# Kernel tuning notes

Hardware: AMD Instinct MI355X
Metric: run time of the kernel (lower is better)

The kernel has to match this reference:

```python
import jax, jax.numpy as jnp
import numpy as np

B, S, H, K = 16, 1024, 1024, 256


def _span(x, Ws, bs, start, end):
    # x: [B,S,H]; start/end: [B,K] int indices into the S axis
    def proj(W, b):
        return jnp.einsum('bsh,oh->bso', x, W) + b  # nn.Linear: x @ W.T + b

    def gather(p, idx):
        # batched index_select along seq axis -> [B,K,H]
        return jnp.take_along_axis(p, idx[..., None], axis=1)

    p1, p2, p3, p4 = (proj(W, b) for W, b in zip(Ws, bs))
    span = (gather(p1, start) + gather(p2, end)
            + (gather(p3, start) - gather(p3, end))
            + gather(p4, start) * gather(p4, end))
    return jnp.tanh(span)


def setup_inputs() -> dict:
    key = jax.random.key(0)
    ks = jax.random.split(key, 20)
    inp = {
        'hidden_states': jax.random.normal(ks[0], (B, S, H), dtype=jnp.float32),
        'prem_word_idxs': jax.random.randint(ks[1], (B, 1, 2, K), 0, S, dtype=jnp.int64) if jax.config.read('jax_enable_x64') else jax.random.randint(ks[1], (B, 1, 2, K), 0, S).astype(jnp.int32),
        'hypo_word_idxs': jax.random.randint(ks[2], (B, 1, 2, K), 0, S).astype(jnp.int32),
    }
    names = ['Wp1', 'bp1', 'Wp2', 'bp2', 'Wp3', 'bp3', 'Wp4', 'bp4',
             'Wh1', 'bh1', 'Wh2', 'bh2', 'Wh3', 'bh3', 'Wh4', 'bh4']
    for i, n in enumerate(names):
        k = ks[3 + i]
        if n.startswith('W'):
            inp[n] = jax.random.normal(k, (H, H), dtype=jnp.float32) * 0.02
        else:
            inp[n] = jax.random.normal(k, (H,), dtype=jnp.float32) * 0.02
    return inp


def reference(hidden_states, prem_word_idxs, hypo_word_idxs,
              Wp1, bp1, Wp2, bp2, Wp3, bp3, Wp4, bp4,
              Wh1, bh1, Wh2, bh2, Wh3, bh3, Wh4, bh4):
    p_idx = prem_word_idxs[:, 0]  # squeeze(1) -> [B,2,K]
    h_idx = hypo_word_idxs[:, 0]
    prem_h_ij = _span(hidden_states, (Wp1, Wp2, Wp3, Wp4), (bp1, bp2, bp3, bp4),
                      p_idx[:, 0], p_idx[:, 1])
    hypo_h_ij = _span(hidden_states, (Wh1, Wh2, Wh3, Wh4), (bh1, bh2, bh3, bh4),
                      h_idx[:, 0], h_idx[:, 1])
    return (prem_h_ij, hypo_h_ij)
```

## Files before the change

kernel.cpp:

```cpp
#include <hip/hip_runtime.h>
#include <hip/hip_bf16.h>

typedef _Float16 f16;
typedef _Float16 f16x4 __attribute__((ext_vector_type(4)));
typedef _Float16 f16x8 __attribute__((ext_vector_type(8)));
typedef float    f32x4 __attribute__((ext_vector_type(4)));

#define H_DIM 1024
#define S_DIM 1024
#define PLANE (1024*1024)
#define MT 128
#define NT 64
#define KT 32
#define AP (MT*KT)
#define ABUF (2*AP)
#define XOFF (6*PLANE)

__device__ __forceinline__ void load_lds16(const f16* g, f16* l) {
    __builtin_amdgcn_global_load_lds(
        (const __attribute__((address_space(1))) void*)g,
        (__attribute__((address_space(3))) void*)l, 16, 0, 0);
}

__global__ __launch_bounds__(256) void prep_w(
    const float* __restrict__ Wp1, const float* __restrict__ Wp2,
    const float* __restrict__ Wp3, const float* __restrict__ Wp4,
    const float* __restrict__ Wh1, const float* __restrict__ Wh2,
    const float* __restrict__ Wh3, const float* __restrict__ Wh4,
    f16* __restrict__ ws)
{
    const int tid  = blockIdx.x * 256 + threadIdx.x;
    const int span = tid >> 18;
    const size_t i = (size_t)(tid & 262143) * 4;
    const float* W1 = span ? Wh1 : Wp1;
    const float* W2 = span ? Wh2 : Wp2;
    const float* W3 = span ? Wh3 : Wp3;
    const float* W4 = span ? Wh4 : Wp4;
    f16* base = ws + (size_t)span * 3 * PLANE;

    f32x4 w1 = *(const f32x4*)(W1 + i);
    f32x4 w2 = *(const f32x4*)(W2 + i);
    f32x4 w3 = *(const f32x4*)(W3 + i);
    f32x4 w4 = *(const f32x4*)(W4 + i);

    f16x4 wa, wb, wc;
#pragma unroll
    for (int j = 0; j < 4; ++j) {
        wa[j] = (f16)(w1[j] + w3[j]);
        wb[j] = (f16)(w2[j] - w3[j]);
        wc[j] = (f16)w4[j];
    }
    *(f16x4*)(base + 0*PLANE + i) = wa;
    *(f16x4*)(base + 1*PLANE + i) = wb;
    *(f16x4*)(base + 2*PLANE + i) = wc;
}

#define XPREP_T (4096*256)
__global__ __launch_bounds__(256) void prep_x(
    const float* __restrict__ x, f16* __restrict__ ws)
{
    const int tid = blockIdx.x * 256 + threadIdx.x;
#pragma unroll
    for (int it = 0; it < 4; ++it) {
        const size_t i = ((size_t)(it * XPREP_T + tid)) * 4;
        f32x4 v = *(const f32x4*)(x + i);
        f16x4 h;
#pragma unroll
        for (int j = 0; j < 4; ++j) h[j] = (f16)v[j];
        *(f16x4*)(ws + XOFF + i) = h;
    }
}

#define K_STEP(FB, FA, WCNT, FIN)                                              \
  {                                                                            \
    f16x8 afr0[4], afr1[4], bfrg[6];                                           \
    const f16* Ab = &A_all[rbA];                                               \
    _Pragma("unroll")                                                          \
    for (int mf = 0; mf < 4; ++mf) {                                           \
      int r = (wm + mf * 16 + lrow) * KT + lqs * 8;                            \
      afr0[mf] = *(const f16x8*)&Ab[r];                                        \
      afr1[mf] = *(const f16x8*)&Ab[AP + r];                                   \
    }                                                                          \
    _Pragma("unroll")                                                          \
    for (int j = 0; j < 6; ++j) {                                              \
      int p = j >> 1, nf = j & 1;                                              \
      bfrg[j] = *(const f16x8*)&B_lds[p * 2048 + (wn + nf * 16 + lrow) * KT + lqs * 8]; \
    }                                                                          \
    if (!(FIN)) {                                                              \
      __asm__ volatile("s_waitcnt lgkmcnt(0)" ::: "memory");                   \
      __builtin_amdgcn_s_barrier();                                            \
      if (FB) {                                                                \
        _Pragma("unroll")                                                      \
        for (int j = 0; j < 3; ++j) { load_lds16(bq[j], &B_lds[bdst[j]]); bq[j] += KT; } \
      }                                                                        \
      if (FA) {                                                                \
        f16* dst = &A_all[wbA];                                                \
        _Pragma("unroll")                                                      \
        for (int j = 0; j < 4; ++j) { load_lds16(ap[j], dst + adst[j]); ap[j] += KT; } \
      }                                                                        \
    }                                                                          \
    _Pragma("unroll")                                                          \
    for (int mf = 0; mf < 4; ++mf)                                             \
      _Pragma("unroll")                                                        \
      for (int nf = 0; nf < 2; ++nf) {                                         \
        accL[mf][nf] = __builtin_amdgcn_mfma_f32_16x16x32_f16(afr0[mf], bfrg[0*2+nf], accL[mf][nf], 0,0,0); \
        accL[mf][nf] = __builtin_amdgcn_mfma_f32_16x16x32_f16(afr1[mf], bfrg[1*2+nf], accL[mf][nf], 0,0,0); \
        accP[mf][nf] = __builtin_amdgcn_mfma_f32_16x16x32_f16(afr0[mf], bfrg[2*2+nf], accP[mf][nf], 0,0,0); \
        accQ[mf][nf] = __builtin_amdgcn_mfma_f32_16x16x32_f16(afr1[mf], bfrg[2*2+nf], accQ[mf][nf], 0,0,0); \
      }                                                                        \
    if (!(FIN)) {                                                              \
      __asm__ volatile("s_waitcnt vmcnt(" #WCNT ")" ::: "memory");             \
      __builtin_amdgcn_s_barrier();                                            \
      rbA = (rbA == 2 * ABUF) ? 0 : rbA + ABUF;                                \
      wbA = (wbA == 2 * ABUF) ? 0 : wbA + ABUF;                                \
    }                                                                          \
  }

__global__ __launch_bounds__(256) void span_gemm(
    const f16* __restrict__ xh,
    const int* __restrict__ idxP, const int* __restrict__ idxH,
    const f16* __restrict__ wpl,
    const float* __restrict__ bp1, const float* __restrict__ bp2, const float* __restrict__ bp4,
    const float* __restrict__ bh1, const float* __restrict__ bh2, const float* __restrict__ bh4,
    float* __restrict__ out)
{
    const int t     = threadIdx.x;
    const int mtile = blockIdx.x;
    const int ntile = blockIdx.y;
    const int span  = blockIdx.z;

    const int* idx   = span ? idxH : idxP;
    const f16* wbase = wpl + (size_t)span * 3 * PLANE;
    const float* b1 = span ? bh1 : bp1;
    const float* b2 = span ? bh2 : bp2;
    const float* b4 = span ? bh4 : bp4;
    float* obase = out + (size_t)span * 4096 * H_DIM;

    __shared__ __align__(16) f16 A_all[3 * ABUF];
    __shared__ __align__(16) f16 B_lds[3 * NT * KT];

    int* rowoff = (int*)A_all;
    {
        int side = t >> 7, m = t & 127;
        int bk = mtile * MT + m;
        int b  = bk >> 8, kk = bk & 255;
        rowoff[side * 128 + m] = (b * S_DIM + idx[b * 512 + side * 256 + kk]) * H_DIM;
    }
    __syncthreads();

    const int wid  = t >> 6;
    const int lane = t & 63;
    const int wm   = (wid & 1) * 64;
    const int wn   = (wid >> 1) * 32;
    const int lrow = lane & 15;
    const int lq   = lane >> 4;
    const int lqs  = lq ^ ((lrow >> 1) & 3);

    const int schunk = (lane & 3) ^ ((lane >> 3) & 3);

    const f16* ap[4]; int adst[4];
#pragma unroll
    for (int j = 0; j < 4; ++j) {
        int o = wid * 4 + j;
        int p = o >> 3, g = o & 7;
        int r = g * 16 + (lane >> 2);
        ap[j]   = xh + rowoff[p * 128 + r] + schunk * 8;
        adst[j] = p * AP + g * 16 * KT;
    }
    __syncthreads();

    const f16* bq[3]; int bdst[3];
#pragma unroll
    for (int j = 0; j < 3; ++j) {
        int o = wid * 3 + j;
        int p = o >> 2, g = o & 3;
        int grow = ntile * NT + g * 16 + (lane >> 2);
        bq[j]   = wbase + (size_t)p * PLANE + (size_t)grow * H_DIM + schunk * 8;
        bdst[j] = p * 2048 + g * 16 * KT;
    }

    f32x4 accL[4][2], accP[4][2], accQ[4][2];
    {
        f32x4 z = {0.f, 0.f, 0.f, 0.f};
#pragma unroll
        for (int mf = 0; mf < 4; ++mf)
#pragma unroll
            for (int nf = 0; nf < 2; ++nf) { accL[mf][nf] = z; accP[mf][nf] = z; accQ[mf][nf] = z; }
    }

#pragma unroll
    for (int j = 0; j < 4; ++j) { load_lds16(ap[j], &A_all[0 * ABUF + adst[j]]); ap[j] += KT; }
#pragma unroll
    for (int j = 0; j < 3; ++j) { load_lds16(bq[j], &B_lds[bdst[j]]); bq[j] += KT; }
#pragma unroll
    for (int j = 0; j < 4; ++j) { load_lds16(ap[j], &A_all[1 * ABUF + adst[j]]); ap[j] += KT; }
    __asm__ volatile("s_waitcnt vmcnt(4)" ::: "memory");
    __builtin_amdgcn_s_barrier();

    int rbA = 0;
    int wbA = 2 * ABUF;

    for (int ks = 0; ks < 30; ++ks) {
        K_STEP(1, 1, 4, 0);
    }
    K_STEP(1, 0, 0, 0);
    K_STEP(0, 0, 0, 1);

#pragma unroll
    for (int mf = 0; mf < 4; ++mf)
#pragma unroll
        for (int nf = 0; nf < 2; ++nf) {
            int col = ntile * NT + wn + nf * 16 + lrow;
            float bb12 = b1[col] + b2[col];
            float bb4  = b4[col];
            int row0 = mtile * MT + wm + mf * 16 + lq * 4;
#pragma unroll
            for (int i = 0; i < 4; ++i) {
                float v = accL[mf][nf][i] + bb12
                        + (accP[mf][nf][i] + bb4) * (accQ[mf][nf][i] + bb4);
                obase[(size_t)(row0 + i) * H_DIM + col] = tanhf(v);
            }
        }
}

extern "C" void kernel_launch(void* const* d_in, const int* in_sizes, int n_in,
                              void* d_out, int out_size, void* d_ws, size_t ws_size,
                              hipStream_t stream) {
    (void)in_sizes; (void)n_in; (void)out_size; (void)ws_size;
    const float* x    = (const float*)d_in[0];
    const int*   idxP = (const int*)d_in[1];
    const int*   idxH = (const int*)d_in[2];
    const float* Wp1 = (const float*)d_in[3];  const float* bp1 = (const float*)d_in[4];
    const float* Wp2 = (const float*)d_in[5];  const float* bp2 = (const float*)d_in[6];
    const float* Wp3 = (const float*)d_in[7];
    const float* Wp4 = (const float*)d_in[9];  const float* bp4 = (const float*)d_in[10];
    const float* Wh1 = (const float*)d_in[11]; const float* bh1 = (const float*)d_in[12];
    const float* Wh2 = (const float*)d_in[13]; const float* bh2 = (const float*)d_in[14];
    const float* Wh3 = (const float*)d_in[15];
    const float* Wh4 = (const float*)d_in[17]; const float* bh4 = (const float*)d_in[18];
    float* out = (float*)d_out;
    f16*   ws  = (f16*)d_ws;

    prep_w<<<2048, 256, 0, stream>>>(Wp1, Wp2, Wp3, Wp4,
                                     Wh1, Wh2, Wh3, Wh4, ws);
    prep_x<<<4096, 256, 0, stream>>>(x, ws);
    span_gemm<<<dim3(32, 16, 2), 256, 0, stream>>>(ws + XOFF, idxP, idxH, ws,
                                                   bp1, bp2, bp4, bh1, bh2, bh4, out);
}
```

Measured before the change: 247.9 us.

## Fuse x fp16 conversion into GEMM, load gathered A rows directly to registers

Drops the prep_x kernel that converted all of hidden_states to fp16. The GEMM now gathers the fp32 rows of x straight from global memory into registers and converts them to fp16 in-kernel. Only the B weights are staged through a double-buffered LDS tile. The warp layout changes to 32 rows by 64 columns per wave, with a launch-bounds occupancy hint of two blocks per SM. This removes a full pass over x and the LDS traffic for A. In exchange it doubles the A bytes read per tile in fp32, duplicates A loads across the 16 N-tiles, and waits on vmcnt(0) every step, which serializes the global loads.

After: 324.5 us. 30.9% more time.

```diff
diff --git a/kernel.cpp b/kernel.cpp
--- a/kernel.cpp
+++ b/kernel.cpp
@@ -1,9 +1,8 @@
 #include <hip/hip_runtime.h>
-#include <hip/hip_bf16.h>
 
 typedef _Float16 f16;
+typedef _Float16 f16x8 __attribute__((ext_vector_type(8)));
 typedef _Float16 f16x4 __attribute__((ext_vector_type(4)));
-typedef _Float16 f16x8 __attribute__((ext_vector_type(8)));
 typedef float    f32x4 __attribute__((ext_vector_type(4)));
 
 #define H_DIM 1024
@@ -12,9 +11,6 @@
 #define MT 128
 #define NT 64
 #define KT 32
-#define AP (MT*KT)
-#define ABUF (2*AP)
-#define XOFF (6*PLANE)
 
 __device__ __forceinline__ void load_lds16(const f16* g, f16* l) {
     __builtin_amdgcn_global_load_lds(
@@ -55,69 +51,61 @@
     *(f16x4*)(base + 2*PLANE + i) = wc;
 }
 
-#define XPREP_T (4096*256)
-__global__ __launch_bounds__(256) void prep_x(
-    const float* __restrict__ x, f16* __restrict__ ws)
-{
-    const int tid = blockIdx.x * 256 + threadIdx.x;
-#pragma unroll
-    for (int it = 0; it < 4; ++it) {
-        const size_t i = ((size_t)(it * XPREP_T + tid)) * 4;
-        f32x4 v = *(const f32x4*)(x + i);
-        f16x4 h;
-#pragma unroll
-        for (int j = 0; j < 4; ++j) h[j] = (f16)v[j];
-        *(f16x4*)(ws + XOFF + i) = h;
-    }
-}
-
-#define K_STEP(FB, FA, WCNT, FIN)                                              \
+#define STEP(CURBUF, CUR, NXT, LAST)                                           \
   {                                                                            \
-    f16x8 afr0[4], afr1[4], bfrg[6];                                           \
-    const f16* Ab = &A_all[rbA];                                               \
+    if (!(LAST)) {                                                             \
+      _Pragma("unroll")                                                        \
+      for (int pl = 0; pl < 2; ++pl)                                           \
+        _Pragma("unroll")                                                      \
+        for (int mf = 0; mf < 2; ++mf) {                                       \
+          const float* s = ab[pl][mf] + KT;                                    \
+          NXT[pl][mf][0] = *(const f32x4*)(s);                                 \
+          NXT[pl][mf][1] = *(const f32x4*)(s + 4);                             \
+        }                                                                      \
+      _Pragma("unroll")                                                        \
+      for (int j = 0; j < 3; ++j)                                              \
+        load_lds16(bq[j] + KT, &B_all[1 - (CURBUF)][bdst[j]]);                 \
+    }                                                                          \
+    f16x8 bf[3][4];                                                            \
     _Pragma("unroll")                                                          \
-    for (int mf = 0; mf < 4; ++mf) {                                           \
-      int r = (wm + mf * 16 + lrow) * KT + lqs * 8;                            \
-      afr0[mf] = *(const f16x8*)&Ab[r];                                        \
-      afr1[mf] = *(const f16x8*)&Ab[AP + r];                                   \
-    }                                                                          \
+    for (int p = 0; p < 3; ++p)                                                \
+      _Pragma("unroll")                                                        \
+      for (int nf = 0; nf < 4; ++nf)                                           \
+        bf[p][nf] = *(const f16x8*)&B_all[CURBUF][p * 2048 +                   \
+                        (nf * 16 + lrow) * KT + lqs * 8];                      \
+    f16x8 af[2][2];                                                            \
     _Pragma("unroll")                                                          \
-    for (int j = 0; j < 6; ++j) {                                              \
-      int p = j >> 1, nf = j & 1;                                              \
-      bfrg[j] = *(const f16x8*)&B_lds[p * 2048 + (wn + nf * 16 + lrow) * KT + lqs * 8]; \
-    }                                                                          \
-    if (!(FIN)) {                                                              \
-      __asm__ volatile("s_waitcnt lgkmcnt(0)" ::: "memory");                   \
+    for (int pl = 0; pl < 2; ++pl)                                             \
+      _Pragma("unroll")                                                        \
+      for (int mf = 0; mf < 2; ++mf)                                           \
+        _Pragma("unroll")                                                      \
+        for (int e = 0; e < 4; ++e) {                                          \
+          af[pl][mf][e]     = (f16)CUR[pl][mf][0][e];                          \
+          af[pl][mf][4 + e] = (f16)CUR[pl][mf][1][e];                          \
+        }                                                                      \
+    _Pragma("unroll")                                                          \
+    for (int mf = 0; mf < 2; ++mf)                                             \
+      _Pragma("unroll")                                                        \
+      for (int nf = 0; nf < 4; ++nf) {                                         \
+        accL[mf][nf] = __builtin_amdgcn_mfma_f32_16x16x32_f16(af[0][mf], bf[0][nf], accL[mf][nf], 0,0,0); \
+        accL[mf][nf] = __builtin_amdgcn_mfma_f32_16x16x32_f16(af[1][mf], bf[1][nf], accL[mf][nf], 0,0,0); \
+        accP[mf][nf] = __builtin_amdgcn_mfma_f32_16x16x32_f16(af[0][mf], bf[2][nf], accP[mf][nf], 0,0,0); \
+        accQ[mf][nf] = __builtin_amdgcn_mfma_f32_16x16x32_f16(af[1][mf], bf[2][nf], accQ[mf][nf], 0,0,0); \
+      }                                                                        \
+    if (!(LAST)) {                                                             \
+      __asm__ volatile("s_waitcnt vmcnt(0)" ::: "memory");                     \
       __builtin_amdgcn_s_barrier();                                            \
-      if (FB) {                                                                \
+      _Pragma("unroll")                                                        \
+      for (int pl = 0; pl < 2; ++pl)                                           \
         _Pragma("unroll")                                                      \
-        for (int j = 0; j < 3; ++j) { load_lds16(bq[j], &B_lds[bdst[j]]); bq[j] += KT; } \
-      }                                                                        \
-      if (FA) {                                                                \
-        f16* dst = &A_all[wbA];                                                \
-        _Pragma("unroll")                                                      \
-        for (int j = 0; j < 4; ++j) { load_lds16(ap[j], dst + adst[j]); ap[j] += KT; } \
-      }                                                                        \
-    }                                                                          \
-    _Pragma("unroll")                                                          \
-    for (int mf = 0; mf < 4; ++mf)                                             \
-      _Pragma("unroll")                                                        \
-      for (int nf = 0; nf < 2; ++nf) {                                         \
-        accL[mf][nf] = __builtin_amdgcn_mfma_f32_16x16x32_f16(afr0[mf], bfrg[0*2+nf], accL[mf][nf], 0,0,0); \
-        accL[mf][nf] = __builtin_amdgcn_mfma_f32_16x16x32_f16(afr1[mf], bfrg[1*2+nf], accL[mf][nf], 0,0,0); \
-        accP[mf][nf] = __builtin_amdgcn_mfma_f32_16x16x32_f16(afr0[mf], bfrg[2*2+nf], accP[mf][nf], 0,0,0); \
-        accQ[mf][nf] = __builtin_amdgcn_mfma_f32_16x16x32_f16(afr1[mf], bfrg[2*2+nf], accQ[mf][nf], 0,0,0); \
-      }                                                                        \
-    if (!(FIN)) {                                                              \
-      __asm__ volatile("s_waitcnt vmcnt(" #WCNT ")" ::: "memory");             \
-      __builtin_amdgcn_s_barrier();                                            \
-      rbA = (rbA == 2 * ABUF) ? 0 : rbA + ABUF;                                \
-      wbA = (wbA == 2 * ABUF) ? 0 : wbA + ABUF;                                \
+        for (int mf = 0; mf < 2; ++mf) ab[pl][mf] += KT;                       \
+      _Pragma("unroll")                                                        \
+      for (int j = 0; j < 3; ++j) bq[j] += KT;                                 \
     }                                                                          \
   }
 
-__global__ __launch_bounds__(256) void span_gemm(
-    const f16* __restrict__ xh,
+__global__ __launch_bounds__(256, 2) void span_gemm(
+    const float* __restrict__ x,
     const int* __restrict__ idxP, const int* __restrict__ idxH,
     const f16* __restrict__ wpl,
     const float* __restrict__ bp1, const float* __restrict__ bp2, const float* __restrict__ bp4,
@@ -136,38 +124,26 @@
     const float* b4 = span ? bh4 : bp4;
     float* obase = out + (size_t)span * 4096 * H_DIM;
 
-    __shared__ __align__(16) f16 A_all[3 * ABUF];
-    __shared__ __align__(16) f16 B_lds[3 * NT * KT];
-
-    int* rowoff = (int*)A_all;
-    {
-        int side = t >> 7, m = t & 127;
-        int bk = mtile * MT + m;
-        int b  = bk >> 8, kk = bk & 255;
-        rowoff[side * 128 + m] = (b * S_DIM + idx[b * 512 + side * 256 + kk]) * H_DIM;
-    }
-    __syncthreads();
+    __shared__ __align__(16) f16 B_all[2][3 * NT * KT];
 
     const int wid  = t >> 6;
     const int lane = t & 63;
-    const int wm   = (wid & 1) * 64;
-    const int wn   = (wid >> 1) * 32;
     const int lrow = lane & 15;
     const int lq   = lane >> 4;
     const int lqs  = lq ^ ((lrow >> 1) & 3);
-
     const int schunk = (lane & 3) ^ ((lane >> 3) & 3);
 
-    const f16* ap[4]; int adst[4];
-#pragma unroll
-    for (int j = 0; j < 4; ++j) {
-        int o = wid * 4 + j;
-        int p = o >> 3, g = o & 7;
-        int r = g * 16 + (lane >> 2);
-        ap[j]   = xh + rowoff[p * 128 + r] + schunk * 8;
-        adst[j] = p * AP + g * 16 * KT;
-    }
-    __syncthreads();
+    const float* ab[2][2];
+#pragma unroll
+    for (int pl = 0; pl < 2; ++pl)
+#pragma unroll
+        for (int mf = 0; mf < 2; ++mf) {
+            int rl = wid * 32 + mf * 16 + lrow;
+            int m  = mtile * MT + rl;
+            int b  = m >> 8, kk = m & 255;
+            int iv = idx[b * 512 + pl * 256 + kk];
+            ab[pl][mf] = x + (size_t)(b * S_DIM + iv) * H_DIM + lq * 8;
+        }
 
     const f16* bq[3]; int bdst[3];
 #pragma unroll
@@ -179,41 +155,42 @@
         bdst[j] = p * 2048 + g * 16 * KT;
     }
 
-    f32x4 accL[4][2], accP[4][2], accQ[4][2];
+    f32x4 accL[2][4], accP[2][4], accQ[2][4];
     {
         f32x4 z = {0.f, 0.f, 0.f, 0.f};
 #pragma unroll
-        for (int mf = 0; mf < 4; ++mf)
-#pragma unroll
-            for (int nf = 0; nf < 2; ++nf) { accL[mf][nf] = z; accP[mf][nf] = z; accQ[mf][nf] = z; }
-    }
-
-#pragma unroll
-    for (int j = 0; j < 4; ++j) { load_lds16(ap[j], &A_all[0 * ABUF + adst[j]]); ap[j] += KT; }
-#pragma unroll
-    for (int j = 0; j < 3; ++j) { load_lds16(bq[j], &B_lds[bdst[j]]); bq[j] += KT; }
-#pragma unroll
-    for (int j = 0; j < 4; ++j) { load_lds16(ap[j], &A_all[1 * ABUF + adst[j]]); ap[j] += KT; }
-    __asm__ volatile("s_waitcnt vmcnt(4)" ::: "memory");
+        for (int mf = 0; mf < 2; ++mf)
+#pragma unroll
+            for (int nf = 0; nf < 4; ++nf) { accL[mf][nf] = z; accP[mf][nf] = z; accQ[mf][nf] = z; }
+    }
+
+    f32x4 a32_0[2][2][2], a32_1[2][2][2];
+#pragma unroll
+    for (int pl = 0; pl < 2; ++pl)
+#pragma unroll
+        for (int mf = 0; mf < 2; ++mf) {
+            a32_0[pl][mf][0] = *(const f32x4*)(ab[pl][mf]);
+            a32_0[pl][mf][1] = *(const f32x4*)(ab[pl][mf] + 4);
+        }
+#pragma unroll
+    for (int j = 0; j < 3; ++j) load_lds16(bq[j], &B_all[0][bdst[j]]);
+    __asm__ volatile("s_waitcnt vmcnt(0)" ::: "memory");
     __builtin_amdgcn_s_barrier();
 
-    int rbA = 0;
-    int wbA = 2 * ABUF;
-
-    for (int ks = 0; ks < 30; ++ks) {
-        K_STEP(1, 1, 4, 0);
-    }
-    K_STEP(1, 0, 0, 0);
-    K_STEP(0, 0, 0, 1);
-
-#pragma unroll
-    for (int mf = 0; mf < 4; ++mf)
-#pragma unroll
-        for (int nf = 0; nf < 2; ++nf) {
-            int col = ntile * NT + wn + nf * 16 + lrow;
+#pragma unroll
+    for (int tt = 0; tt < 16; ++tt) {
+        STEP(0, a32_0, a32_1, 0);
+        STEP(1, a32_1, a32_0, (tt == 15));
+    }
+
+#pragma unroll
+    for (int mf = 0; mf < 2; ++mf)
+#pragma unroll
+        for (int nf = 0; nf < 4; ++nf) {
+            int col = ntile * NT + nf * 16 + lrow;
             float bb12 = b1[col] + b2[col];
             float bb4  = b4[col];
-            int row0 = mtile * MT + wm + mf * 16 + lq * 4;
+            int row0 = mtile * MT + wid * 32 + mf * 16 + lq * 4;
 #pragma unroll
             for (int i = 0; i < 4; ++i) {
                 float v = accL[mf][nf][i] + bb12
@@ -243,7 +220,6 @@
 
     prep_w<<<2048, 256, 0, stream>>>(Wp1, Wp2, Wp3, Wp4,
                                      Wh1, Wh2, Wh3, Wh4, ws);
-    prep_x<<<4096, 256, 0, stream>>>(x, ws);
-    span_gemm<<<dim3(32, 16, 2), 256, 0, stream>>>(ws + XOFF, idxP, idxH, ws,
+    span_gemm<<<dim3(32, 16, 2), 256, 0, stream>>>(x, idxP, idxH, ws,
                                                    bp1, bp2, bp4, bh1, bh2, bh4, out);
 }
```
